# Performance work log

Hardware: AMD Instinct MI355X
Metric: run time of the kernel (lower is better)

Reference implementation:

```python
import jax, jax.numpy as jnp
import numpy as np

D_MODEL = 1024
N_HEADS = 16
D_HEAD = D_MODEL // N_HEADS
BATCH = 2
SEQ = 2048


def setup_inputs() -> dict:
    key = jax.random.key(0)
    ks = jax.random.split(key, 16)
    s = 0.02
    d = D_MODEL
    return {
        "x": jax.random.normal(ks[0], (BATCH, SEQ, d), jnp.float32),
        "Wq": jax.random.normal(ks[1], (d, d), jnp.float32) * s,
        "bq": jnp.zeros((d,), jnp.float32),
        "Wk": jax.random.normal(ks[2], (d, d), jnp.float32) * s,
        "bk": jnp.zeros((d,), jnp.float32),
        "Wv": jax.random.normal(ks[3], (d, d), jnp.float32) * s,
        "bv": jnp.zeros((d,), jnp.float32),
        "Wo": jax.random.normal(ks[4], (d, d), jnp.float32) * s,
        "bo": jnp.zeros((d,), jnp.float32),
        "Wt": jax.random.normal(ks[5], (d, 1), jnp.float32) * s,
        "bt": jnp.zeros((1,), jnp.float32),
        "Wg": jax.random.normal(ks[6], (d, d), jnp.float32) * s,
        "bg": jnp.zeros((d,), jnp.float32),
    }


def _evolved_attention(x, Wq, bq, Wk, bk, Wv, bv, Wo, bo, Wt, bt, Wg, bg):
    B, S, D = x.shape
    H, dh = N_HEADS, D_HEAD

    def heads(y):  # [B,S,D] -> [B,H,S,dh]
        return y.reshape(B, S, H, dh).transpose(0, 2, 1, 3)

    q = heads(x @ Wq + bq)
    k = heads(x @ Wk + bk)
    v = heads(x @ Wv + bv)

    # cosine similarity (F.normalize with eps=1e-12)
    qn = q / jnp.maximum(jnp.linalg.norm(q, axis=-1, keepdims=True), 1e-12)
    kn = k / jnp.maximum(jnp.linalg.norm(k, axis=-1, keepdims=True), 1e-12)
    scores = jnp.einsum("bhqd,bhkd->bhqk", qn, kn)

    # adaptive temperature: sigmoid(temp_proj(mean_s x)) + 0.5, shape [B,1]
    temp = jax.nn.sigmoid(x.mean(axis=1) @ Wt + bt) + 0.5  # [B,1]
    scores = scores / temp[:, None, None, :]  # broadcast [B,1,1,1]

    # sparsemax-style: softmax over top-k (k = S//4), scattered back
    kk = max(1, S // 4)
    vals, idx = jax.lax.top_k(scores, kk)          # [B,H,S,kk]
    w = jax.nn.softmax(vals, axis=-1)
    rows = jnp.arange(B * H * S)[:, None]
    attn = (
        jnp.zeros((B * H * S, S), scores.dtype)
        .at[rows, idx.reshape(-1, kk)]
        .set(w.reshape(-1, kk))
        .reshape(B, H, S, S)
    )

    out = jnp.einsum("bhqk,bhkd->bhqd", attn, v)
    out = out.transpose(0, 2, 1, 3).reshape(B, S, D)
    out = out @ Wo + bo

    # highway gating
    gate = jax.nn.sigmoid(x @ Wg + bg)
    return gate * out + (1.0 - gate) * x


def reference(x, Wq, bq, Wk, bk, Wv, bv, Wo, bo, Wt, bt, Wg, bg):
    return _evolved_attention(x, Wq, bq, Wk, bk, Wv, bv, Wo, bo, Wt, bt, Wg, bg)
```

## Files before the change

### kernel.cpp

```cpp
#include <hip/hip_runtime.h>

typedef unsigned short u16;
typedef __attribute__((ext_vector_type(4))) float f32x4;
typedef __attribute__((ext_vector_type(8))) short bf16x8;
typedef __attribute__((ext_vector_type(4))) int i32x4;

#define BB 2
#define SS 2048
#define DD 1024
#define HH 16
#define DH 64
#define KK 512

#define OFF_SCAL  ((size_t)0)
#define OFF_WT    ((size_t)256)
#define OFF_XB    (OFF_WT + (size_t)5*1024*1024*2)
#define OFF_AO    OFF_XB
#define OFF_QH    (OFF_XB + (size_t)4096*1024*2)
#define OFF_QN    (OFF_QH + (size_t)4096*4096*2)
#define OFF_KN    (OFF_QN + (size_t)4096*1024*2)
#define OFF_VT    (OFF_KN + (size_t)4096*1024*2)

__device__ __forceinline__ float b2f(u16 u) { return __uint_as_float(((unsigned)u) << 16); }
__device__ __forceinline__ u16 f2b(float f) {
    unsigned u = __float_as_uint(f);
    return (u16)((u + 0x7fffu + ((u >> 16) & 1u)) >> 16);
}

__device__ __forceinline__ void gload16(const u16* g, u16* l) {
    __builtin_amdgcn_global_load_lds(
        (__attribute__((address_space(1))) void*)g,
        (__attribute__((address_space(3))) void*)l, 16, 0, 0);
}

__global__ __launch_bounds__(256) void convert_x(const float* x, u16* xb) {
    int i = (blockIdx.x * 256 + threadIdx.x) * 4;
    float4 v = *(const float4*)(x + i);
    u16 r0 = f2b(v.x), r1 = f2b(v.y), r2 = f2b(v.z), r3 = f2b(v.w);
    xb[i] = r0; xb[i + 1] = r1; xb[i + 2] = r2; xb[i + 3] = r3;
}

__global__ __launch_bounds__(256) void transpose_w(
        const float* Wq, const float* Wk, const float* Wv, const float* Wg, const float* Wo,
        u16* WT) {
    int z = blockIdx.z;
    const float* src = (z == 0) ? Wq : (z == 1) ? Wk : (z == 2) ? Wv : (z == 3) ? Wg : Wo;
    u16* dst = WT + (size_t)z * 1024 * 1024;
    __shared__ float tile[64][65];
    int n0 = blockIdx.x * 64, k0 = blockIdx.y * 64;
    int rbase = threadIdx.x >> 6, c = threadIdx.x & 63;
#pragma unroll
    for (int i = 0; i < 16; i++) {
        int r = i * 4 + rbase;
        tile[r][c] = src[(size_t)(k0 + r) * 1024 + n0 + c];
    }
    __syncthreads();
#pragma unroll
    for (int i = 0; i < 16; i++) {
        int r = i * 4 + rbase;
        dst[(size_t)(n0 + r) * 1024 + k0 + c] = f2b(tile[c][r]);
    }
}

__global__ __launch_bounds__(256) void temp_partial(const float* x, const float* Wt,
                                                    float* accbuf) {
    int b = blockIdx.x >> 7, ch = blockIdx.x & 127;
    float a = 0.f;
    for (int si = 0; si < 16; si++) {
        int s = ch * 16 + si;
        const float* xr = x + ((size_t)(b * SS + s)) * DD;
#pragma unroll
        for (int k = 0; k < 4; k++) {
            int c = threadIdx.x + k * 256;
            a += xr[c] * Wt[c];
        }
    }
    for (int o = 32; o; o >>= 1) a += __shfl_xor(a, o);
    __shared__ float red[4];
    if ((threadIdx.x & 63) == 0) red[threadIdx.x >> 6] = a;
    __syncthreads();
    if (threadIdx.x == 0) atomicAdd(&accbuf[b], red[0] + red[1] + red[2] + red[3]);
}

__global__ void temp_final(const float* accbuf, const float* bt, float* itemp) {
    int t = threadIdx.x;
    if (t < BB) {
        float v = accbuf[t] / (float)SS + bt[0];
        float tmp = 1.f / (1.f + __expf(-v)) + 0.5f;
        itemp[t] = 1.f / tmp;
    }
}

__global__ __launch_bounds__(256) void gemm_qkvg(
        const u16* X, const u16* WT,
        const float* bq, const float* bk, const float* bv, const float* bg, u16* Qh) {
    __shared__ __align__(16) u16 la[128 * 32];
    __shared__ __align__(16) u16 lb[128 * 32];
    int tid = threadIdx.x, wid = tid >> 6, lane = tid & 63;
    int quad = lane >> 4, ml = lane & 15;
    int m0 = blockIdx.x * 128, n0 = blockIdx.y * 128;
    int wr = wid >> 1, wc = wid & 1;

    f32x4 acc[4][4];
#pragma unroll
    for (int i = 0; i < 4; i++)
#pragma unroll
        for (int j = 0; j < 4; j++) acc[i][j] = (f32x4){0.f, 0.f, 0.f, 0.f};

    int t0 = wid * 2, t1 = t0 + 1;
    int r0 = lane >> 2, kp = lane & 3;
    const u16* ga0 = X + (size_t)(m0 + t0 * 16 + r0) * 1024 + kp * 8;
    const u16* ga1 = X + (size_t)(m0 + t1 * 16 + r0) * 1024 + kp * 8;
    const u16* gb0 = WT + (size_t)(n0 + t0 * 16 + r0) * 1024 + kp * 8;
    const u16* gb1 = WT + (size_t)(n0 + t1 * 16 + r0) * 1024 + kp * 8;
    u16* la0 = la + t0 * 512; u16* la1 = la + t1 * 512;
    u16* lb0 = lb + t0 * 512; u16* lb1 = lb + t1 * 512;

    for (int k0 = 0; k0 < 1024; k0 += 32) {
        gload16(ga0 + k0, la0);
        gload16(ga1 + k0, la1);
        gload16(gb0 + k0, lb0);
        gload16(gb1 + k0, lb1);
        __syncthreads();
        bf16x8 af[4], bfr[4];
#pragma unroll
        for (int mi = 0; mi < 4; mi++)
            af[mi] = *(const bf16x8*)&la[(wr * 64 + mi * 16 + ml) * 32 + quad * 8];
#pragma unroll
        for (int ni = 0; ni < 4; ni++)
            bfr[ni] = *(const bf16x8*)&lb[(wc * 64 + ni * 16 + ml) * 32 + quad * 8];
#pragma unroll
        for (int mi = 0; mi < 4; mi++)
#pragma unroll
            for (int ni = 0; ni < 4; ni++)
                acc[mi][ni] = __builtin_amdgcn_mfma_f32_16x16x32_bf16(af[mi], bfr[ni],
                                                                      acc[mi][ni], 0, 0, 0);
        __syncthreads();
    }

#pragma unroll
    for (int mi = 0; mi < 4; mi++)
#pragma unroll
        for (int ni = 0; ni < 4; ni++) {
            int col = n0 + wc * 64 + ni * 16 + ml;
            int mat = col >> 10, bc = col & 1023;
            const float* bp = (mat == 0) ? bq : (mat == 1) ? bk : (mat == 2) ? bv : bg;
            float bias = bp[bc];
#pragma unroll
            for (int r = 0; r < 4; r++) {
                int row = m0 + wr * 64 + mi * 16 + quad * 4 + r;
                Qh[(size_t)row * 4096 + col] = f2b(acc[mi][ni][r] + bias);
            }
        }
}

__global__ __launch_bounds__(256) void norm_repack(const u16* Qh, u16* qn, u16* kn, u16* vt) {
    __shared__ u16 vtile[64][66];
    int bid = blockIdx.x;
    int bh = bid >> 5, st = bid & 31;
    int b = bh >> 4, h = bh & 15;
    int s0 = st * 64;
    int tid = threadIdx.x, wid = tid >> 6, lane = tid & 63;

    for (int i = 0; i < 16; i++) {
        int tt = i * 4 + wid;
        int s = s0 + tt;
        const u16* rowp = Qh + (size_t)(b * SS + s) * 4096 + h * 64;
        float q = b2f(rowp[lane]);
        float k = b2f(rowp[1024 + lane]);
        u16 v = rowp[2048 + lane];
        float sq = q * q, sk = k * k;
#pragma unroll
        for (int o = 32; o; o >>= 1) { sq += __shfl_xor(sq, o); sk += __shfl_xor(sk, o); }
        float qd = fmaxf(sqrtf(sq), 1e-12f), kd = fmaxf(sqrtf(sk), 1e-12f);
        qn[((size_t)bh * SS + s) * DH + lane] = f2b(q / qd);
        kn[((size_t)bh * SS + s) * DH + lane] = f2b(k / kd);
        vtile[lane][tt] = v;
    }
    __syncthreads();

#pragma unroll
    for (int p = 0; p < 2; p++) {
        int d = p * 32 + wid * 8 + (lane >> 3);
        int sc = lane & 7;
        const u16* src = &vtile[d][sc * 8];
        unsigned w0 = *(const unsigned*)(src);
        unsigned w1 = *(const unsigned*)(src + 2);
        unsigned w2 = *(const unsigned*)(src + 4);
        unsigned w3 = *(const unsigned*)(src + 6);
        i32x4 out4 = (i32x4){(int)w0, (int)w1, (int)w2, (int)w3};
        *(i32x4*)(vt + ((size_t)bh * DH + d) * SS + s0 + sc * 8) = out4;
    }
}

#define EST 2088

__global__ __launch_bounds__(1024, 8) void attn_kernel(
        const u16* qn, const u16* kn, const u16* vt, const float* itemp, u16* ao) {
    __shared__ __align__(16) u16 e16[16 * EST];
    __shared__ float pvp[3][16][66];
    __shared__ float zrow_s[16];

    int tid = threadIdx.x, wid = tid >> 6, lane = tid & 63;
    int quad = lane >> 4, nl = lane & 15;
    int bid = blockIdx.x;
    int swz = (bid & 7) * 512 + (bid >> 3);
    int bh = swz >> 7, qt = swz & 127;
    int b = bh >> 4, h = bh & 15;
    const u16* qbase = qn + ((size_t)bh * SS + qt * 16) * DH;
    const u16* kbase = kn + (size_t)bh * SS * DH;
    const u16* vbase = vt + (size_t)bh * DH * SS;
    float it = itemp[b];

    bf16x8 aq0 = *(const bf16x8*)(qbase + nl * DH + quad * 8);
    bf16x8 aq1 = *(const bf16x8*)(qbase + nl * DH + 32 + quad * 8);

#pragma unroll 4
    for (int c = 0; c < 8; c++) {
        int j = c * 256 + wid * 16 + nl;
        const u16* kr = kbase + (size_t)j * DH;
        bf16x8 b0 = *(const bf16x8*)(kr + quad * 8);
        bf16x8 b1 = *(const bf16x8*)(kr + 32 + quad * 8);
        f32x4 acc = (f32x4){0.f, 0.f, 0.f, 0.f};
        __builtin_amdgcn_s_setprio(1);
        acc = __builtin_amdgcn_mfma_f32_16x16x32_bf16(aq0, b0, acc, 0, 0, 0);
        acc = __builtin_amdgcn_mfma_f32_16x16x32_bf16(aq1, b1, acc, 0, 0, 0);
        __builtin_amdgcn_s_setprio(0);
#pragma unroll
        for (int r = 0; r < 4; r++) e16[(quad * 4 + r) * EST + j] = f2b(acc[r] * it);
    }
    __syncthreads();

    {
        u16* rp = &e16[wid * EST];
        int kk[32];
#pragma unroll
        for (int i = 0; i < 4; i++) {
            i32x4 kv = *(const i32x4*)(rp + i * 512 + lane * 8);
#pragma unroll
            for (int j = 0; j < 4; j++) {
                unsigned r2 = (unsigned)kv[j];
                unsigned t = ((r2 >> 15) & 0x00010001u) * 0x7FFFu;
                unsigned key2 = r2 ^ 0x80008000u ^ t;
                int lo = (int)(key2 & 0xFFFFu), hi = (int)(key2 >> 16);
                asm volatile("v_mov_b32 %0, %1" : "=v"(kk[i * 8 + j * 2]) : "v"(lo));
                asm volatile("v_mov_b32 %0, %1" : "=v"(kk[i * 8 + j * 2 + 1]) : "v"(hi));
            }
        }

        int P = 0;
        for (int bit = 15; bit >= 0; bit--) {
            int cand = P | (1 << bit);
            int c0 = 0, c1 = 0, c2 = 0, c3 = 0;
#pragma unroll
            for (int c = 0; c < 32; c += 4) {
                c0 += (int)__popcll(__ballot(kk[c] >= cand));
                c1 += (int)__popcll(__ballot(kk[c + 1] >= cand));
                c2 += (int)__popcll(__ballot(kk[c + 2] >= cand));
                c3 += (int)__popcll(__ballot(kk[c + 3] >= cand));
            }
            int cnt = (c0 + c1) + (c2 + c3);
            if (cnt >= KK) P = cand;
            if (cnt == KK) break;
        }

        float z = 0.f;
#pragma unroll
        for (int i = 0; i < 4; i++) {
            i32x4 ev;
#pragma unroll
            for (int j = 0; j < 4; j++) {
                int k0i = kk[i * 8 + j * 2], k1i = kk[i * 8 + j * 2 + 1];
                unsigned r0 = (unsigned)k0i ^ ((k0i & 0x8000) ? 0x8000u : 0xFFFFu);
                unsigned r1 = (unsigned)k1i ^ ((k1i & 0x8000) ? 0x8000u : 0xFFFFu);
                float f0 = __uint_as_float(r0 << 16);
                float f1 = __uint_as_float(r1 << 16);
                float e0 = (k0i >= P) ? __expf(f0) : 0.f;
                float e1 = (k1i >= P) ? __expf(f1) : 0.f;
                z += e0 + e1;
                int pw;
                asm("v_cvt_pk_bf16_f32 %0, %1, %2" : "=v"(pw) : "v"(e0), "v"(e1));
                ev[j] = pw;
            }
            *(i32x4*)(rp + i * 512 + lane * 8) = ev;
        }
#pragma unroll
        for (int o = 32; o; o >>= 1) z += __shfl_xor(z, o);
        if (lane == 0) zrow_s[wid] = z;
    }
    __syncthreads();

    f32x4 accp = (f32x4){0.f, 0.f, 0.f, 0.f};
    int kq = wid >> 2, g = wid & 3;
    int dh = g * 16 + nl;
    const u16* vrow = vbase + (size_t)dh * SS;
#pragma unroll 4
    for (int c = 0; c < 8; c++) {
        int j0 = kq * 512 + c * 64;
#pragma unroll
        for (int ks = 0; ks < 2; ks++) {
            bf16x8 a = *(const bf16x8*)&e16[nl * EST + j0 + ks * 32 + quad * 8];
            bf16x8 bfr = *(const bf16x8*)(vrow + j0 + ks * 32 + quad * 8);
            __builtin_amdgcn_s_setprio(1);
            accp = __builtin_amdgcn_mfma_f32_16x16x32_bf16(a, bfr, accp, 0, 0, 0);
            __builtin_amdgcn_s_setprio(0);
        }
    }
    if (kq) {
#pragma unroll
        for (int r = 0; r < 4; r++) pvp[kq - 1][quad * 4 + r][dh] = accp[r];
    }
    __syncthreads();
    if (kq == 0) {
#pragma unroll
        for (int r = 0; r < 4; r++) {
            int q = quad * 4 + r;
            float val = (accp[r] + pvp[0][q][dh] + pvp[1][q][dh] + pvp[2][q][dh]) / zrow_s[q];
            size_t row = (size_t)(b * SS + qt * 16 + q);
            ao[row * DD + h * 64 + dh] = f2b(val);
        }
    }
}

__global__ __launch_bounds__(256) void gemm_out(
        const u16* AO, const u16* WTo, const float* bo,
        const u16* Qh, const float* x, float* out) {
    __shared__ __align__(16) u16 la[128 * 32];
    __shared__ __align__(16) u16 lb[128 * 32];
    int tid = threadIdx.x, wid = tid >> 6, lane = tid & 63;
    int quad = lane >> 4, ml = lane & 15;
    int m0 = blockIdx.x * 128, n0 = blockIdx.y * 128;
    int wr = wid >> 1, wc = wid & 1;

    f32x4 acc[4][4];
#pragma unroll
    for (int i = 0; i < 4; i++)
#pragma unroll
        for (int j = 0; j < 4; j++) acc[i][j] = (f32x4){0.f, 0.f, 0.f, 0.f};

    int t0 = wid * 2, t1 = t0 + 1;
    int r0 = lane >> 2, kp = lane & 3;
    const u16* ga0 = AO + (size_t)(m0 + t0 * 16 + r0) * 1024 + kp * 8;
    const u16* ga1 = AO + (size_t)(m0 + t1 * 16 + r0) * 1024 + kp * 8;
    const u16* gb0 = WTo + (size_t)(n0 + t0 * 16 + r0) * 1024 + kp * 8;
    const u16* gb1 = WTo + (size_t)(n0 + t1 * 16 + r0) * 1024 + kp * 8;
    u16* la0 = la + t0 * 512; u16* la1 = la + t1 * 512;
    u16* lb0 = lb + t0 * 512; u16* lb1 = lb + t1 * 512;

    for (int k0 = 0; k0 < 1024; k0 += 32) {
        gload16(ga0 + k0, la0);
        gload16(ga1 + k0, la1);
        gload16(gb0 + k0, lb0);
        gload16(gb1 + k0, lb1);
        __syncthreads();
        bf16x8 af[4], bfr[4];
#pragma unroll
        for (int mi = 0; mi < 4; mi++)
            af[mi] = *(const bf16x8*)&la[(wr * 64 + mi * 16 + ml) * 32 + quad * 8];
#pragma unroll
        for (int ni = 0; ni < 4; ni++)
            bfr[ni] = *(const bf16x8*)&lb[(wc * 64 + ni * 16 + ml) * 32 + quad * 8];
#pragma unroll
        for (int mi = 0; mi < 4; mi++)
#pragma unroll
            for (int ni = 0; ni < 4; ni++)
                acc[mi][ni] = __builtin_amdgcn_mfma_f32_16x16x32_bf16(af[mi], bfr[ni],
                                                                      acc[mi][ni], 0, 0, 0);
        __syncthreads();
    }

#pragma unroll
    for (int mi = 0; mi < 4; mi++)
#pragma unroll
        for (int ni = 0; ni < 4; ni++) {
            int col = n0 + wc * 64 + ni * 16 + ml;
            float bias = bo[col];
#pragma unroll
            for (int r = 0; r < 4; r++) {
                int row = m0 + wr * 64 + mi * 16 + quad * 4 + r;
                float gv = b2f(Qh[(size_t)row * 4096 + 3072 + col]);
                float gate = 1.f / (1.f + __expf(-gv));
                float xv = x[(size_t)row * 1024 + col];
                float o = acc[mi][ni][r] + bias;
                out[(size_t)row * 1024 + col] = gate * o + (1.f - gate) * xv;
            }
        }
}

extern "C" void kernel_launch(void* const* d_in, const int* in_sizes, int n_in,
                              void* d_out, int out_size, void* d_ws, size_t ws_size,
                              hipStream_t stream) {
    const float* x  = (const float*)d_in[0];
    const float* Wq = (const float*)d_in[1];
    const float* bq = (const float*)d_in[2];
    const float* Wk = (const float*)d_in[3];
    const float* bk = (const float*)d_in[4];
    const float* Wv = (const float*)d_in[5];
    const float* bv = (const float*)d_in[6];
    const float* Wo = (const float*)d_in[7];
    const float* bo = (const float*)d_in[8];
    const float* Wt = (const float*)d_in[9];
    const float* bt = (const float*)d_in[10];
    const float* Wg = (const float*)d_in[11];
    const float* bg = (const float*)d_in[12];

    char* w = (char*)d_ws;
    float* accbuf = (float*)(w + OFF_SCAL);
    float* itemp  = accbuf + 2;
    u16*   WT     = (u16*)(w + OFF_WT);
    u16*   xb     = (u16*)(w + OFF_XB);
    u16*   ao     = (u16*)(w + OFF_AO);
    u16*   Qh     = (u16*)(w + OFF_QH);
    u16*   qn     = (u16*)(w + OFF_QN);
    u16*   kn     = (u16*)(w + OFF_KN);
    u16*   vt     = (u16*)(w + OFF_VT);

    hipMemsetAsync(accbuf, 0, 2 * sizeof(float), stream);

    convert_x<<<4096, 256, 0, stream>>>(x, xb);
    transpose_w<<<dim3(16, 16, 5), 256, 0, stream>>>(Wq, Wk, Wv, Wg, Wo, WT);
    temp_partial<<<256, 256, 0, stream>>>(x, Wt, accbuf);
    temp_final<<<1, 64, 0, stream>>>(accbuf, bt, itemp);
    gemm_qkvg<<<dim3(32, 32), 256, 0, stream>>>(xb, WT, bq, bk, bv, bg, Qh);
    norm_repack<<<1024, 256, 0, stream>>>(Qh, qn, kn, vt);
    attn_kernel<<<4096, 1024, 0, stream>>>(qn, kn, vt, itemp, ao);
    gemm_out<<<dim3(32, 8), 256, 0, stream>>>(ao, WT + (size_t)4 * 1024 * 1024, bo, Qh, x,
                                              (float*)d_out);
}
```

Baseline: 489.8 us.

## Replace bitwise radix top-k threshold search with interpolation/bisection over quantized keys

Scaled bf16 scores (bounded by cosine/temperature) are mapped to 16-bit fixed-point keys packed two per register. The top-k threshold is then found by alternating interpolation and bisection steps instead of a fixed 16-bit MSB radix search. This aims to cut the number of wave-wide ballot passes and halve the register footprint of the key array. In exchange, the quantization assumes scores stay within about ±2, relies on keys with ties at a coarser granularity than bf16, and reloads scores from LDS in the exp pass.

```diff
diff --git a/kernel.cpp b/kernel.cpp
--- a/kernel.cpp
+++ b/kernel.cpp
@@ -233,50 +233,64 @@
 
     {
         u16* rp = &e16[wid * EST];
-        int kk[32];
+        const float SC = 16000.0f, OF = 32768.0f;
+        unsigned pk[16];
 #pragma unroll
         for (int i = 0; i < 4; i++) {
             i32x4 kv = *(const i32x4*)(rp + i * 512 + lane * 8);
 #pragma unroll
             for (int j = 0; j < 4; j++) {
                 unsigned r2 = (unsigned)kv[j];
-                unsigned t = ((r2 >> 15) & 0x00010001u) * 0x7FFFu;
-                unsigned key2 = r2 ^ 0x80008000u ^ t;
-                int lo = (int)(key2 & 0xFFFFu), hi = (int)(key2 >> 16);
-                asm volatile("v_mov_b32 %0, %1" : "=v"(kk[i * 8 + j * 2]) : "v"(lo));
-                asm volatile("v_mov_b32 %0, %1" : "=v"(kk[i * 8 + j * 2 + 1]) : "v"(hi));
-            }
-        }
-
-        int P = 0;
-        for (int bit = 15; bit >= 0; bit--) {
-            int cand = P | (1 << bit);
-            int c0 = 0, c1 = 0, c2 = 0, c3 = 0;
-#pragma unroll
-            for (int c = 0; c < 32; c += 4) {
-                c0 += (int)__popcll(__ballot(kk[c] >= cand));
-                c1 += (int)__popcll(__ballot(kk[c + 1] >= cand));
-                c2 += (int)__popcll(__ballot(kk[c + 2] >= cand));
-                c3 += (int)__popcll(__ballot(kk[c + 3] >= cand));
-            }
-            int cnt = (c0 + c1) + (c2 + c3);
-            if (cnt >= KK) P = cand;
-            if (cnt == KK) break;
-        }
+                unsigned u0 = (unsigned)fmaf(__uint_as_float(r2 << 16), SC, OF);
+                unsigned u1 = (unsigned)fmaf(__uint_as_float(r2 & 0xFFFF0000u), SC, OF);
+                pk[i * 4 + j] = u0 | (u1 << 16);
+            }
+        }
+
+        int lo = 447, cntLo = 2048;
+        int hi = 65089, cntHi = 0;
+        for (int itr = 0; itr < 32 && hi - lo > 1; ++itr) {
+            int cand;
+            if (itr & 1) {
+                cand = (lo + hi) >> 1;
+            } else {
+                float fr = (float)(cntLo - KK) / (float)(cntLo - cntHi);
+                cand = lo + (int)(fr * (float)(hi - lo));
+                cand = min(max(cand, lo + 1), hi - 1);
+            }
+            unsigned ch = ((unsigned)cand) << 16;
+            int c0 = 0, c1 = 0;
+#pragma unroll
+            for (int i = 0; i < 16; i += 2) {
+                c0 += (int)__popcll(__ballot(pk[i] >= ch));
+                c0 += (int)__popcll(__ballot((pk[i] << 16) >= ch));
+                c1 += (int)__popcll(__ballot(pk[i + 1] >= ch));
+                c1 += (int)__popcll(__ballot((pk[i + 1] << 16) >= ch));
+            }
+            int cnt = c0 + c1;
+            if (cnt >= KK) {
+                lo = cand; cntLo = cnt;
+                if (cnt == KK) break;
+            } else {
+                hi = cand; cntHi = cnt;
+            }
+        }
+        unsigned P = (unsigned)lo;
 
         float z = 0.f;
 #pragma unroll
         for (int i = 0; i < 4; i++) {
+            i32x4 kv = *(const i32x4*)(rp + i * 512 + lane * 8);
             i32x4 ev;
 #pragma unroll
             for (int j = 0; j < 4; j++) {
-                int k0i = kk[i * 8 + j * 2], k1i = kk[i * 8 + j * 2 + 1];
-                unsigned r0 = (unsigned)k0i ^ ((k0i & 0x8000) ? 0x8000u : 0xFFFFu);
-                unsigned r1 = (unsigned)k1i ^ ((k1i & 0x8000) ? 0x8000u : 0xFFFFu);
-                float f0 = __uint_as_float(r0 << 16);
-                float f1 = __uint_as_float(r1 << 16);
-                float e0 = (k0i >= P) ? __expf(f0) : 0.f;
-                float e1 = (k1i >= P) ? __expf(f1) : 0.f;
+                unsigned r2 = (unsigned)kv[j];
+                float f0 = __uint_as_float(r2 << 16);
+                float f1 = __uint_as_float(r2 & 0xFFFF0000u);
+                unsigned u0 = (unsigned)fmaf(f0, SC, OF);
+                unsigned u1 = (unsigned)fmaf(f1, SC, OF);
+                float e0 = (u0 >= P) ? __expf(f0) : 0.f;
+                float e1 = (u1 >= P) ? __expf(f1) : 0.f;
                 z += e0 + e1;
                 int pw;
                 asm("v_cvt_pk_bf16_f32 %0, %1, %2" : "=v"(pw) : "v"(e0), "v"(e1));
```

Result: slower. 509.1 us (+4.0%).

## Merge prep kernels into one launch and swizzle GEMM block order

Applied to the files above, without the earlier changes.

Folds convert_x, transpose_w and temp_partial into a single prep kernel that dispatches on block index, and moves the temp_final computation into block 0 of norm_repack. This cuts three kernel launches and the gaps between them. Both GEMMs also remap block indices so that groups of eight consecutive blocks share weight tiles, aiming for better L2 reuse. The fused prep kernel's __syncthreads sits inside divergent but block-uniform branches, so it remains safe.

```diff
diff --git a/kernel.cpp b/kernel.cpp
--- a/kernel.cpp
+++ b/kernel.cpp
@@ -33,61 +33,54 @@
         (__attribute__((address_space(3))) void*)l, 16, 0, 0);
 }
 
-__global__ __launch_bounds__(256) void convert_x(const float* x, u16* xb) {
-    int i = (blockIdx.x * 256 + threadIdx.x) * 4;
-    float4 v = *(const float4*)(x + i);
-    u16 r0 = f2b(v.x), r1 = f2b(v.y), r2 = f2b(v.z), r3 = f2b(v.w);
-    xb[i] = r0; xb[i + 1] = r1; xb[i + 2] = r2; xb[i + 3] = r3;
-}
-
-__global__ __launch_bounds__(256) void transpose_w(
-        const float* Wq, const float* Wk, const float* Wv, const float* Wg, const float* Wo,
-        u16* WT) {
-    int z = blockIdx.z;
-    const float* src = (z == 0) ? Wq : (z == 1) ? Wk : (z == 2) ? Wv : (z == 3) ? Wg : Wo;
-    u16* dst = WT + (size_t)z * 1024 * 1024;
+__global__ __launch_bounds__(256) void prep(
+        const float* x, const float* Wq, const float* Wk, const float* Wv,
+        const float* Wg, const float* Wo, const float* Wt,
+        u16* xb, u16* WT, float* accbuf) {
     __shared__ float tile[64][65];
-    int n0 = blockIdx.x * 64, k0 = blockIdx.y * 64;
-    int rbase = threadIdx.x >> 6, c = threadIdx.x & 63;
-#pragma unroll
-    for (int i = 0; i < 16; i++) {
-        int r = i * 4 + rbase;
-        tile[r][c] = src[(size_t)(k0 + r) * 1024 + n0 + c];
-    }
-    __syncthreads();
-#pragma unroll
-    for (int i = 0; i < 16; i++) {
-        int r = i * 4 + rbase;
-        dst[(size_t)(n0 + r) * 1024 + k0 + c] = f2b(tile[c][r]);
-    }
-}
-
-__global__ __launch_bounds__(256) void temp_partial(const float* x, const float* Wt,
-                                                    float* accbuf) {
-    int b = blockIdx.x >> 7, ch = blockIdx.x & 127;
-    float a = 0.f;
-    for (int si = 0; si < 16; si++) {
-        int s = ch * 16 + si;
-        const float* xr = x + ((size_t)(b * SS + s)) * DD;
-#pragma unroll
-        for (int k = 0; k < 4; k++) {
-            int c = threadIdx.x + k * 256;
-            a += xr[c] * Wt[c];
-        }
-    }
-    for (int o = 32; o; o >>= 1) a += __shfl_xor(a, o);
-    __shared__ float red[4];
-    if ((threadIdx.x & 63) == 0) red[threadIdx.x >> 6] = a;
-    __syncthreads();
-    if (threadIdx.x == 0) atomicAdd(&accbuf[b], red[0] + red[1] + red[2] + red[3]);
-}
-
-__global__ void temp_final(const float* accbuf, const float* bt, float* itemp) {
-    int t = threadIdx.x;
-    if (t < BB) {
-        float v = accbuf[t] / (float)SS + bt[0];
-        float tmp = 1.f / (1.f + __expf(-v)) + 0.5f;
-        itemp[t] = 1.f / tmp;
+    int bid = blockIdx.x;
+    if (bid < 4096) {
+        int i = (bid * 256 + threadIdx.x) * 4;
+        float4 v = *(const float4*)(x + i);
+        u16 r0 = f2b(v.x), r1 = f2b(v.y), r2 = f2b(v.z), r3 = f2b(v.w);
+        xb[i] = r0; xb[i + 1] = r1; xb[i + 2] = r2; xb[i + 3] = r3;
+    } else if (bid < 5376) {
+        int t = bid - 4096;
+        int z = t >> 8, xy = t & 255;
+        const float* src = (z == 0) ? Wq : (z == 1) ? Wk : (z == 2) ? Wv
+                         : (z == 3) ? Wg : Wo;
+        u16* dst = WT + (size_t)z * 1024 * 1024;
+        int n0 = (xy & 15) * 64, k0 = (xy >> 4) * 64;
+        int rbase = threadIdx.x >> 6, c = threadIdx.x & 63;
+#pragma unroll
+        for (int i = 0; i < 16; i++) {
+            int r = i * 4 + rbase;
+            tile[r][c] = src[(size_t)(k0 + r) * 1024 + n0 + c];
+        }
+        __syncthreads();
+#pragma unroll
+        for (int i = 0; i < 16; i++) {
+            int r = i * 4 + rbase;
+            dst[(size_t)(n0 + r) * 1024 + k0 + c] = f2b(tile[c][r]);
+        }
+    } else {
+        int t = bid - 5376;
+        int b = t >> 7, ch = t & 127;
+        float a = 0.f;
+        for (int si = 0; si < 16; si++) {
+            int s = ch * 16 + si;
+            const float* xr = x + ((size_t)(b * SS + s)) * DD;
+#pragma unroll
+            for (int k = 0; k < 4; k++) {
+                int c = threadIdx.x + k * 256;
+                a += xr[c] * Wt[c];
+            }
+        }
+        for (int o = 32; o; o >>= 1) a += __shfl_xor(a, o);
+        __shared__ float red[4];
+        if ((threadIdx.x & 63) == 0) red[threadIdx.x >> 6] = a;
+        __syncthreads();
+        if (threadIdx.x == 0) atomicAdd(&accbuf[b], red[0] + red[1] + red[2] + red[3]);
     }
 }
 
@@ -98,7 +91,9 @@
     __shared__ __align__(16) u16 lb[128 * 32];
     int tid = threadIdx.x, wid = tid >> 6, lane = tid & 63;
     int quad = lane >> 4, ml = lane & 15;
-    int m0 = blockIdx.x * 128, n0 = blockIdx.y * 128;
+    int lid = blockIdx.y * 32 + blockIdx.x;
+    int swz = (lid & 7) * 128 + (lid >> 3);
+    int m0 = (swz & 31) * 128, n0 = (swz >> 5) * 128;
     int wr = wid >> 1, wc = wid & 1;
 
     f32x4 acc[4][4];
@@ -154,9 +149,16 @@
         }
 }
 
-__global__ __launch_bounds__(256) void norm_repack(const u16* Qh, u16* qn, u16* kn, u16* vt) {
+__global__ __launch_bounds__(256) void norm_repack(const u16* Qh, const float* accbuf,
+                                                   const float* bt, float* itemp,
+                                                   u16* qn, u16* kn, u16* vt) {
     __shared__ u16 vtile[64][66];
     int bid = blockIdx.x;
+    if (bid == 0 && threadIdx.x < BB) {
+        float v = accbuf[threadIdx.x] / (float)SS + bt[0];
+        float tmp = 1.f / (1.f + __expf(-v)) + 0.5f;
+        itemp[threadIdx.x] = 1.f / tmp;
+    }
     int bh = bid >> 5, st = bid & 31;
     int b = bh >> 4, h = bh & 15;
     int s0 = st * 64;
@@ -329,7 +331,9 @@
     __shared__ __align__(16) u16 lb[128 * 32];
     int tid = threadIdx.x, wid = tid >> 6, lane = tid & 63;
     int quad = lane >> 4, ml = lane & 15;
-    int m0 = blockIdx.x * 128, n0 = blockIdx.y * 128;
+    int lid = blockIdx.y * 32 + blockIdx.x;
+    int swz = (lid & 7) * 32 + (lid >> 3);
+    int m0 = (swz & 31) * 128, n0 = (swz >> 5) * 128;
     int wr = wid >> 1, wc = wid & 1;
 
     f32x4 acc[4][4];
@@ -417,12 +421,9 @@
 
     hipMemsetAsync(accbuf, 0, 2 * sizeof(float), stream);
 
-    convert_x<<<4096, 256, 0, stream>>>(x, xb);
-    transpose_w<<<dim3(16, 16, 5), 256, 0, stream>>>(Wq, Wk, Wv, Wg, Wo, WT);
-    temp_partial<<<256, 256, 0, stream>>>(x, Wt, accbuf);
-    temp_final<<<1, 64, 0, stream>>>(accbuf, bt, itemp);
+    prep<<<5632, 256, 0, stream>>>(x, Wq, Wk, Wv, Wg, Wo, Wt, xb, WT, accbuf);
     gemm_qkvg<<<dim3(32, 32), 256, 0, stream>>>(xb, WT, bq, bk, bv, bg, Qh);
-    norm_repack<<<1024, 256, 0, stream>>>(Qh, qn, kn, vt);
+    norm_repack<<<1024, 256, 0, stream>>>(Qh, accbuf, bt, itemp, qn, kn, vt);
     attn_kernel<<<4096, 1024, 0, stream>>>(qn, kn, vt, itemp, ao);
     gemm_out<<<dim3(32, 8), 256, 0, stream>>>(ao, WT + (size_t)4 * 1024 * 1024, bo, Qh, x,
                                               (float*)d_out);
```

Measured after the change: 488.4 us (median of 2 runs). No clear change (-0.3%).
